# Kernel optimization log

Measured on AMD Instinct MI355X. Metric: run time of the kernel, lower is better.

Reference implementation:

```python
import jax, jax.numpy as jnp
import numpy as np

B = 4            # batch
L = 4096         # max_len
D_MODEL = 1024   # qkv_dim == out_features
H = 16           # num_heads
SEG = 64         # max_seg_len
HD = D_MODEL // H          # head_dim = 64
NSEG = L // SEG            # num segments = 64
NEG = -1e10


def setup_inputs() -> dict:
    key = jax.random.key(0)
    k0, k1, k2, k3, k4 = jax.random.split(key, 5)
    scale = 1.0 / np.sqrt(D_MODEL).astype(np.float32)
    x = jax.random.normal(k0, (B, L, D_MODEL), jnp.float32)
    wq = jax.random.normal(k1, (D_MODEL, H, HD), jnp.float32) * scale
    wk = jax.random.normal(k2, (D_MODEL, H, HD), jnp.float32) * scale
    wv = jax.random.normal(k3, (D_MODEL, H, HD), jnp.float32) * scale
    wo = jax.random.normal(k4, (H, HD, D_MODEL), jnp.float32) * scale
    return {"input_qkv": x, "wq": wq, "wk": wk, "wv": wv, "wo": wo}


def reference(input_qkv, wq, wk, wv, wo):
    inv_sqrt_hd = 1.0 / np.sqrt(HD).astype(np.float32)
    # QKV projections; query pre-scaled by 1/sqrt(head_dim) as in get_qkv
    q = jnp.einsum('bld,dhf->blhf', input_qkv, wq) * inv_sqrt_hd
    k = jnp.einsum('bld,dhf->blhf', input_qkv, wk)
    v = jnp.einsum('bld,dhf->blhf', input_qkv, wv)

    cq = q.reshape(B * NSEG, SEG, H, HD)
    ck = k.reshape(B * NSEG, SEG, H, HD)
    cv = v.reshape(B * NSEG, SEG, H, HD)

    # Pooled per-segment query attends over its own segment's keys/values.
    # Original: merged_query = max(cq)*sqrt(HD), then flax dot_product_attention
    # rescales by 1/sqrt(HD) -> the two scalings cancel, so use max(cq) directly.
    mq = jnp.max(cq, axis=1, keepdims=True)                    # [B*NSEG, 1, H, HD]
    s_logits = jnp.einsum('bqhd,bkhd->bhqk', mq, ck)
    s_w = jax.nn.softmax(s_logits, axis=-1)
    s = jnp.einsum('bhqk,bkhd->bqhd', s_w, cv)                  # [B*NSEG, 1, H, HD]
    span_val = s.reshape(B, NSEG, H, HD)
    span_key = jnp.max(ck, axis=1).reshape(B, NSEG, H, HD)

    # Local causal attention logits within each segment
    causal = jnp.tril(jnp.ones((SEG, SEG), bool))
    local_bias = jnp.where(causal, 0.0, NEG).astype(jnp.float32)[None, :, None, :]
    local_logits = jnp.einsum('bqhd,bkhd->bqhk', cq, ck) + local_bias
    local_logits = local_logits.reshape(B, L, H, SEG)

    # Cross-segment logits: each token attends to strictly earlier segment summaries
    seg_id = jnp.arange(NSEG)
    prev_bias = jnp.where(seg_id[:, None] > seg_id[None, :], 0.0, NEG).astype(jnp.float32)
    prev_bias = jnp.repeat(prev_bias, SEG, axis=0)[None, :, None, :]  # [1, L, 1, NSEG]
    prev_logits = jnp.einsum('bqhd,bkhd->bqhk', q, span_key) + prev_bias

    # Joint softmax over [local keys | previous-segment summaries]
    joint = jnp.concatenate([local_logits, prev_logits], axis=-1)   # [B, L, H, SEG+NSEG]
    w = jax.nn.softmax(joint, axis=-1)
    local_att = w[..., :SEG].reshape(B * NSEG, SEG, H, SEG)
    prev_att = w[..., SEG:]

    local_merged = jnp.einsum('bqhk,bkhd->bqhd', local_att, cv).reshape(B, L, H, HD)
    prev_merged = jnp.einsum('bqhk,bkhd->bqhd', prev_att, span_val)

    return jnp.einsum('blhd,hdf->blf', local_merged + prev_merged, wo)
```

## Files before the change

### kernel.cpp

```cpp
#include <hip/hip_runtime.h>

#define BB    4
#define LL    4096
#define DM    1024
#define HH    16
#define SEGC  64
#define HDC   64
#define NSEGC 64
#define NEGV  -1.0e10f

typedef __bf16 bf16x8 __attribute__((ext_vector_type(8)));
typedef float  f32x4  __attribute__((ext_vector_type(4)));

__device__ __forceinline__ float bf2f(unsigned short s) {
  union { unsigned int u; float f; } x; x.u = ((unsigned int)s) << 16; return x.f;
}
__device__ __forceinline__ unsigned short f2bf(float f) {
  union { float f; unsigned int u; } x; x.f = f;
  unsigned int u = x.u;
  return (unsigned short)((u + 0x7fffu + ((u >> 16) & 1u)) >> 16);
}

__device__ __forceinline__ void gl2lds16(const unsigned short* g, unsigned short* l) {
  __builtin_amdgcn_global_load_lds(
      (const __attribute__((address_space(1))) unsigned int*)g,
      (__attribute__((address_space(3))) unsigned int*)l,
      16, 0, 0);
}

__device__ __forceinline__ void g2lds16(unsigned short* dst, const unsigned short* src) {
  int4 a = *(const int4*)(src);
  int4 b = *(const int4*)(src + 8);
  unsigned int* d = (unsigned int*)dst;
  const unsigned int* pa = (const unsigned int*)&a;
  const unsigned int* pb = (const unsigned int*)&b;
  d[0]=pa[0]; d[1]=pa[1]; d[2]=pa[2]; d[3]=pa[3];
  d[4]=pb[0]; d[5]=pb[1]; d[6]=pb[2]; d[7]=pb[3];
}

__global__ __launch_bounds__(256) void cvt_x(const float* __restrict__ x,
                                             unsigned short* __restrict__ xb) {
  const size_t i = ((size_t)blockIdx.x * 256 + threadIdx.x) * 8;
  float4 a = *(const float4*)(x + i);
  float4 b = *(const float4*)(x + i + 4);
  unsigned short o[8];
  o[0]=f2bf(a.x); o[1]=f2bf(a.y); o[2]=f2bf(a.z); o[3]=f2bf(a.w);
  o[4]=f2bf(b.x); o[5]=f2bf(b.y); o[6]=f2bf(b.z); o[7]=f2bf(b.w);
  *(int4*)(xb + i) = *(const int4*)o;
}

__global__ __launch_bounds__(256) void transpose_w(
    const float* __restrict__ wq, const float* __restrict__ wk,
    const float* __restrict__ wv, const float* __restrict__ wo,
    unsigned short* __restrict__ WqkvT, unsigned short* __restrict__ woT) {
  __shared__ unsigned short TS[64 * 65];

  const int z  = blockIdx.z;
  const int bx = blockIdx.x;
  const int by = blockIdx.y;
  const int t  = threadIdx.x;

  const float* src; unsigned short* dst; float scale = 1.0f;
  if (z == 0)      { src = wq; dst = WqkvT;               scale = 0.125f; }
  else if (z == 1) { src = wk; dst = WqkvT + 1024 * 1024; }
  else if (z == 2) { src = wv; dst = WqkvT + 2048 * 1024; }
  else             { src = wo; dst = woT; }

  const int rr = t >> 4;
  const int c4 = (t & 15) * 4;
  #pragma unroll
  for (int it = 0; it < 4; it++) {
    const int r = it * 16 + rr;
    float4 f = *(const float4*)(src + (size_t)(by * 64 + r) * 1024 + bx * 64 + c4);
    TS[(c4 + 0) * 65 + r] = f2bf(f.x * scale);
    TS[(c4 + 1) * 65 + r] = f2bf(f.y * scale);
    TS[(c4 + 2) * 65 + r] = f2bf(f.z * scale);
    TS[(c4 + 3) * 65 + r] = f2bf(f.w * scale);
  }
  __syncthreads();

  const int wr = t >> 3;
  const int w8 = (t & 7) * 8;
  #pragma unroll
  for (int it = 0; it < 2; it++) {
    const int n = it * 32 + wr;
    unsigned short o[8];
    #pragma unroll
    for (int j = 0; j < 8; j++) o[j] = TS[n * 65 + w8 + j];
    *(int4*)(dst + (size_t)(bx * 64 + n) * 1024 + by * 64 + w8) = *(const int4*)o;
  }
}

template <bool C_F32>
__global__ __launch_bounds__(512, 2) void gemm256(
    const unsigned short* __restrict__ A,
    const unsigned short* __restrict__ Bt,
    void* __restrict__ Cv,
    int ldc)
{
  __shared__ __align__(16) unsigned short L[2][2][4][4096];

  const int t    = threadIdx.x;
  const int wave = t >> 6;
  const int lane = t & 63;
  const int l15  = lane & 15;
  const int q4   = lane >> 4;
  const int wm   = wave >> 2;
  const int wn   = wave & 3;

  const int nwg = gridDim.x;
  const int wg  = blockIdx.x;
  const int swz = (wg & 7) * (nwg >> 3) + (wg >> 3);
  const int m0  = (swz & 63) << 8;
  const int n0  = (swz >> 6) << 8;

  const int srow = ((wave >> 1) << 4) + (lane >> 2);
  const int scol = ((wave & 1) << 5) + (((lane & 3) << 3) ^ (((lane >> 5) & 1) << 4));
  const size_t laneoff = (size_t)srow * 1024 + scol;
  const unsigned short* Ab = A  + (size_t)m0 * 1024 + laneoff;
  const unsigned short* Bb = Bt + (size_t)n0 * 1024 + laneoff;

  const int rdoff = l15 * 32 + ((q4 * 8) ^ (((l15 >> 3) & 1) << 4));

#define SA_(d, q, kt) gl2lds16(Ab + ((size_t)(q) * 64) * 1024 + (size_t)(kt) * 64, \
                               &L[d][0][q][0] + wave * 512)
#define SB_(d, q, kt) gl2lds16(Bb + ((size_t)(q) * 64) * 1024 + (size_t)(kt) * 64, \
                               &L[d][1][q][0] + wave * 512)
#define LDA8(d, i, kk) (*(const bf16x8*)(&L[d][0][wm * 2 + ((i) >> 2)][0] + \
                        ((((i) & 3) * 2 + (kk)) * 512) + rdoff))
#define LDB8(d, j, kk) (*(const bf16x8*)(&L[d][1][wn][0] + \
                        ((((j) * 2 + (kk))) * 512) + rdoff))
#define BAR()   asm volatile("s_barrier" ::: "memory")
#define VMW(n)  asm volatile("s_waitcnt vmcnt(" #n ")" ::: "memory")
#define MFMA_(av, bv, cv) __builtin_amdgcn_mfma_f32_16x16x32_bf16(av, bv, cv, 0, 0, 0)

  bf16x8 aLo[4][2], aHi[4][2], b01e[2][2], b01o[2][2], b23[2][2];

#define RD_ALO(d) { _Pragma("unroll") for (int ii = 0; ii < 4; ++ii) { \
    aLo[ii][0] = LDA8(d, ii, 0); aLo[ii][1] = LDA8(d, ii, 1); } }
#define RD_AHI(d) { _Pragma("unroll") for (int ii = 0; ii < 4; ++ii) { \
    aHi[ii][0] = LDA8(d, 4 + ii, 0); aHi[ii][1] = LDA8(d, 4 + ii, 1); } }
#define RD_B01(d, ARR) { _Pragma("unroll") for (int jj = 0; jj < 2; ++jj) { \
    ARR[jj][0] = LDB8(d, jj, 0); ARR[jj][1] = LDB8(d, jj, 1); } }
#define RD_B23(d) { _Pragma("unroll") for (int jj = 0; jj < 2; ++jj) { \
    b23[jj][0] = LDB8(d, 2 + jj, 0); b23[jj][1] = LDB8(d, 2 + jj, 1); } }

#define CL(AR, BR, IO, J0) do { \
    __builtin_amdgcn_sched_barrier(0); \
    __builtin_amdgcn_s_setprio(1); \
    _Pragma("unroll") for (int ii = 0; ii < 4; ++ii) { \
      _Pragma("unroll") for (int jj = 0; jj < 2; ++jj) { \
        acc[(IO) + ii][(J0) + jj] = MFMA_(AR[ii][0], BR[jj][0], acc[(IO) + ii][(J0) + jj]); \
        acc[(IO) + ii][(J0) + jj] = MFMA_(AR[ii][1], BR[jj][1], acc[(IO) + ii][(J0) + jj]); \
      } } \
    __builtin_amdgcn_s_setprio(0); } while (0)

  f32x4 acc[8][4];
  #pragma unroll
  for (int i = 0; i < 8; ++i)
    #pragma unroll
    for (int j = 0; j < 4; ++j) acc[i][j] = (f32x4){0.f, 0.f, 0.f, 0.f};

  SA_(0,0,0); SA_(0,2,0); SB_(0,0,0); SB_(0,1,0); SB_(0,2,0); SB_(0,3,0);
  SA_(0,1,0); SA_(0,3,0);
  SA_(1,0,1); SA_(1,2,1); SB_(1,0,1); SB_(1,1,1); SB_(1,2,1); SB_(1,3,1);
  SA_(1,1,1); SA_(1,3,1);
  VMW(8); BAR();
  RD_ALO(0); RD_B01(0, b01e);

  #pragma unroll 1
  for (int it = 0; it < 8; ++it) {
    const int t2 = (2 * it + 2) & 15;
    const int t3 = (2 * it + 3) & 15;

    RD_B23(0);
    SA_(0, 0, t2); SA_(0, 2, t2);
    CL(aLo, b01e, 0, 0);
    BAR();

    RD_AHI(0);
    SB_(0, 0, t2); SB_(0, 1, t2);
    CL(aLo, b23, 0, 2);
    BAR();

    SB_(0, 2, t2); SB_(0, 3, t2);
    CL(aHi, b23, 4, 2);
    VMW(6); BAR();

    RD_ALO(1); RD_B01(1, b01o);
    SA_(0, 1, t2); SA_(0, 3, t2);
    CL(aHi, b01e, 4, 0);
    BAR();

    RD_B23(1);
    SA_(1, 0, t3); SA_(1, 2, t3);
    CL(aLo, b01o, 0, 0);
    BAR();

    RD_AHI(1);
    SB_(1, 0, t3); SB_(1, 1, t3);
    CL(aLo, b23, 0, 2);
    BAR();

    SB_(1, 2, t3); SB_(1, 3, t3);
    CL(aHi, b23, 4, 2);
    VMW(6); BAR();

    RD_ALO(0); RD_B01(0, b01e);
    SA_(1, 1, t3); SA_(1, 3, t3);
    CL(aHi, b01o, 4, 0);
    BAR();
  }

  #pragma unroll
  for (int i = 0; i < 8; ++i) {
    #pragma unroll
    for (int j = 0; j < 4; ++j) {
      const int col = n0 + wn * 64 + j * 16 + l15;
      #pragma unroll
      for (int r = 0; r < 4; ++r) {
        const int row = m0 + wm * 128 + i * 16 + q4 * 4 + r;
        if (C_F32) ((float*)Cv)[(size_t)row * ldc + col] = acc[i][j][r];
        else ((unsigned short*)Cv)[(size_t)row * ldc + col] = f2bf(acc[i][j][r]);
      }
    }
  }
  VMW(0);

#undef SA_
#undef SB_
#undef LDA8
#undef LDB8
#undef BAR
#undef VMW
#undef MFMA_
#undef RD_ALO
#undef RD_AHI
#undef RD_B01
#undef RD_B23
#undef CL
}

__global__ __launch_bounds__(64) void span_kernel(
    const unsigned short* __restrict__ qkv,
    unsigned short* __restrict__ spanK,
    unsigned short* __restrict__ spanV)
{
  __shared__ unsigned short QS[64 * 66], KS[64 * 66], VS[64 * 66];
  __shared__ float mqs[64], ws[64];

  const int c = blockIdx.x;
  const int h = blockIdx.y;
  const int b = c >> 6, n = c & 63;
  const int t = threadIdx.x;

  const size_t rowbase = ((size_t)(b * LL + n * SEGC + t)) * 3072 + h * 64;
  #pragma unroll
  for (int j = 0; j < 4; j++) {
    g2lds16(QS + t * 66 + j * 16, qkv + rowbase + j * 16);
    g2lds16(KS + t * 66 + j * 16, qkv + rowbase + 1024 + j * 16);
    g2lds16(VS + t * 66 + j * 16, qkv + rowbase + 2048 + j * 16);
  }
  __syncthreads();

  float mqa = -3.0e38f, mqb = -3.0e38f, ska = -3.0e38f, skc = -3.0e38f;
  #pragma unroll 8
  for (int r = 0; r < 64; r += 2) {
    mqa = fmaxf(mqa, bf2f(QS[r * 66 + t]));
    mqb = fmaxf(mqb, bf2f(QS[(r + 1) * 66 + t]));
    ska = fmaxf(ska, bf2f(KS[r * 66 + t]));
    skc = fmaxf(skc, bf2f(KS[(r + 1) * 66 + t]));
  }
  mqs[t] = fmaxf(mqa, mqb);
  spanK[((size_t)c * 16 + h) * 64 + t] = f2bf(fmaxf(ska, skc));
  __syncthreads();

  float l0 = 0.f, l1 = 0.f;
  #pragma unroll 8
  for (int d = 0; d < 64; d += 2) {
    l0 += mqs[d] * bf2f(KS[t * 66 + d]);
    l1 += mqs[d + 1] * bf2f(KS[t * 66 + d + 1]);
  }
  float logit = l0 + l1;
  float m = logit;
  #pragma unroll
  for (int off = 32; off; off >>= 1) m = fmaxf(m, __shfl_xor(m, off, 64));
  float e = __expf(logit - m);
  float s = e;
  #pragma unroll
  for (int off = 32; off; off >>= 1) s += __shfl_xor(s, off, 64);
  ws[t] = e / s;
  __syncthreads();

  float sv0 = 0.f, sv1 = 0.f;
  #pragma unroll 8
  for (int kk = 0; kk < 64; kk += 2) {
    sv0 += ws[kk] * bf2f(VS[kk * 66 + t]);
    sv1 += ws[kk + 1] * bf2f(VS[(kk + 1) * 66 + t]);
  }
  spanV[((size_t)c * 16 + h) * 64 + t] = f2bf(sv0 + sv1);
}

__global__ __launch_bounds__(256) void attn_kernel(
    const unsigned short* __restrict__ qkv,
    const unsigned short* __restrict__ spanK,
    const unsigned short* __restrict__ spanV,
    unsigned short* __restrict__ att)
{
  __shared__ unsigned short VT[64 * 136];
  __shared__ unsigned short WL[64 * 136];

  const int c = blockIdx.x;
  const int h = blockIdx.y;
  const int b = c >> 6, n = c & 63;
  const int t = threadIdx.x;
  const int wave = t >> 6;
  const int lane = t & 63;
  const int l15  = lane & 15;
  const int q4   = lane >> 4;

  #pragma unroll
  for (int it = 0; it < 4; it++) {
    const int idx = t + 256 * it;
    const int kp  = idx >> 3;
    const int fc  = (idx & 7) * 8;
    const unsigned short* src;
    if (kp < 64)
      src = qkv + ((size_t)(b * LL + n * SEGC + kp)) * 3072 + 2048 + h * 64 + fc;
    else
      src = spanV + ((size_t)(b * 64 + (kp - 64)) * 16 + h) * 64 + fc;
    int4 val = *(const int4*)src;
    const unsigned short* e = (const unsigned short*)&val;
    const int kb = kp >> 3;
    #pragma unroll
    for (int i = 0; i < 8; i++) {
      const int f  = fc + i;
      const int nb = (kb & 8) | ((kb ^ (f >> 3)) & 7);
      VT[f * 136 + nb * 8 + (kp & 7)] = e[i];
    }
  }

  bf16x8 af[2];
  {
    const size_t qbase = ((size_t)(b * LL + n * SEGC + wave * 16 + l15)) * 3072
                         + h * 64 + q4 * 8;
    af[0] = *(const bf16x8*)(qkv + qbase);
    af[1] = *(const bf16x8*)(qkv + qbase + 32);
  }

  f32x4 accl[8];
  #pragma unroll
  for (int tt = 0; tt < 8; tt++) accl[tt] = (f32x4){0.f, 0.f, 0.f, 0.f};

  #pragma unroll
  for (int s = 0; s < 2; s++) {
    bf16x8 bfr[8];
    #pragma unroll
    for (int tt = 0; tt < 8; tt++) {
      const unsigned short* src;
      if (tt < 4)
        src = qkv + ((size_t)(b * LL + n * SEGC + tt * 16 + l15)) * 3072
              + 1024 + h * 64 + s * 32 + q4 * 8;
      else
        src = spanK + ((size_t)((b * 64 + (tt - 4) * 16 + l15) * 16 + h)) * 64
              + s * 32 + q4 * 8;
      bfr[tt] = *(const bf16x8*)src;
    }
    #pragma unroll
    for (int tt = 0; tt < 8; tt++)
      accl[tt] = __builtin_amdgcn_mfma_f32_16x16x32_bf16(af[s], bfr[tt], accl[tt], 0, 0, 0);
  }

  #pragma unroll
  for (int tt = 0; tt < 8; tt++) {
    const int col = (tt & 3) * 16 + l15;
    #pragma unroll
    for (int rr = 0; rr < 4; rr++) {
      const int r_att = wave * 16 + q4 * 4 + rr;
      const bool valid = (tt < 4) ? (col <= r_att) : (col < n);
      if (!valid) accl[tt][rr] = NEGV;
    }
  }

  #pragma unroll
  for (int rr = 0; rr < 4; rr++) {
    float mx = accl[0][rr];
    #pragma unroll
    for (int tt = 1; tt < 8; tt++) mx = fmaxf(mx, accl[tt][rr]);
    #pragma unroll
    for (int msk = 1; msk < 16; msk <<= 1) mx = fmaxf(mx, __shfl_xor(mx, msk, 64));
    float sm = 0.f;
    float ex[8];
    #pragma unroll
    for (int tt = 0; tt < 8; tt++) { ex[tt] = __expf(accl[tt][rr] - mx); sm += ex[tt]; }
    #pragma unroll
    for (int msk = 1; msk < 16; msk <<= 1) sm += __shfl_xor(sm, msk, 64);
    const float inv = 1.0f / sm;
    const int r_att = wave * 16 + q4 * 4 + rr;
    #pragma unroll
    for (int tt = 0; tt < 8; tt++) {
      const int colj = (tt < 4) ? (tt * 16 + l15) : (64 + (tt - 4) * 16 + l15);
      WL[r_att * 136 + colj] = f2bf(ex[tt] * inv);
    }
  }

  __syncthreads();

  f32x4 accm[4];
  #pragma unroll
  for (int j = 0; j < 4; j++) accm[j] = (f32x4){0.f, 0.f, 0.f, 0.f};
  #pragma unroll
  for (int s = 0; s < 4; s++) {
    const bf16x8 aw = *(const bf16x8*)(WL + (wave * 16 + l15) * 136 + s * 32 + q4 * 8);
    #pragma unroll
    for (int j = 0; j < 4; j++) {
      const int f  = j * 16 + l15;
      const int kb = s * 4 + q4;
      const int nb = (kb & 8) | ((kb ^ (f >> 3)) & 7);
      const bf16x8 bv = *(const bf16x8*)(VT + f * 136 + nb * 8);
      accm[j] = __builtin_amdgcn_mfma_f32_16x16x32_bf16(aw, bv, accm[j], 0, 0, 0);
    }
  }

  #pragma unroll
  for (int j = 0; j < 4; j++) {
    #pragma unroll
    for (int rr = 0; rr < 4; rr++) {
      const int row = wave * 16 + q4 * 4 + rr;
      const int col = j * 16 + l15;
      att[((size_t)(b * LL + n * SEGC + row)) * 1024 + h * 64 + col] = f2bf(accm[j][rr]);
    }
  }
}

extern "C" void kernel_launch(void* const* d_in, const int* in_sizes, int n_in,
                              void* d_out, int out_size, void* d_ws, size_t ws_size,
                              hipStream_t stream) {
  const float* x  = (const float*)d_in[0];
  const float* wq = (const float*)d_in[1];
  const float* wk = (const float*)d_in[2];
  const float* wv = (const float*)d_in[3];
  const float* wo = (const float*)d_in[4];
  float* out = (float*)d_out;

  unsigned short* wsp   = (unsigned short*)d_ws;
  unsigned short* xb    = wsp;
  unsigned short* qkv   = xb + 16777216;
  unsigned short* WqkvT = qkv + 50331648;
  unsigned short* woT   = WqkvT + 3145728;
  unsigned short* skb   = woT + 1048576;
  unsigned short* svb   = skb + 262144;
  unsigned short* attb  = xb;

  cvt_x<<<8192, 256, 0, stream>>>(x, xb);
  transpose_w<<<dim3(16, 16, 4), 256, 0, stream>>>(wq, wk, wv, wo, WqkvT, woT);
  gemm256<false><<<768, 512, 0, stream>>>(xb, WqkvT, (void*)qkv, 3072);
  span_kernel<<<dim3(256, 16), 64, 0, stream>>>(qkv, skb, svb);
  attn_kernel<<<dim3(256, 16), 256, 0, stream>>>(qkv, skb, svb, attb);
  gemm256<true><<<256, 512, 0, stream>>>(attb, woT, (void*)out, 1024);
}
```

Before: 346.4 us.

## Retile GEMMs to 128x256 blocks and stage attention keys in LDS

Replaces the 256x256, BK=64 hand-scheduled GEMM with a 128x256 tile using BK=32, a simple double-buffered loop and an XCD-aware block mapping. This doubles the grid for both the QKV and output projections, aiming at better CU fill, especially for the small output GEMM. The trade-off is less data reuse per tile and more barriers per unit of work. Separately, the attention kernel now loads segment keys and span keys into a padded LDS buffer once, instead of each wave issuing strided global loads for its MFMA operands.

```diff
diff --git a/kernel.cpp b/kernel.cpp
--- a/kernel.cpp
+++ b/kernel.cpp
@@ -92,13 +92,14 @@
 }
 
 template <bool C_F32>
-__global__ __launch_bounds__(512, 2) void gemm256(
+__global__ __launch_bounds__(512, 4) void gemm128x256(
     const unsigned short* __restrict__ A,
     const unsigned short* __restrict__ Bt,
     void* __restrict__ Cv,
     int ldc)
 {
-  __shared__ __align__(16) unsigned short L[2][2][4][4096];
+  __shared__ __align__(16) unsigned short LA[2][8][512];
+  __shared__ __align__(16) unsigned short LB[2][16][512];
 
   const int t    = threadIdx.x;
   const int wave = t >> 6;
@@ -108,118 +109,76 @@
   const int wm   = wave >> 2;
   const int wn   = wave & 3;
 
-  const int nwg = gridDim.x;
   const int wg  = blockIdx.x;
-  const int swz = (wg & 7) * (nwg >> 3) + (wg >> 3);
-  const int m0  = (swz & 63) << 8;
-  const int n0  = (swz >> 6) << 8;
-
-  const int srow = ((wave >> 1) << 4) + (lane >> 2);
-  const int scol = ((wave & 1) << 5) + (((lane & 3) << 3) ^ (((lane >> 5) & 1) << 4));
-  const size_t laneoff = (size_t)srow * 1024 + scol;
-  const unsigned short* Ab = A  + (size_t)m0 * 1024 + laneoff;
-  const unsigned short* Bb = Bt + (size_t)n0 * 1024 + laneoff;
+  const int xcd = wg & 7;
+  const int r_  = wg >> 3;
+  const int lm  = r_ & 15;
+  const int nt  = r_ >> 4;
+  const int m0  = ((xcd << 4) + lm) << 7;
+  const int n0  = nt << 8;
+
+  const int srow = lane >> 2;
+  const int scol = ((lane & 3) << 3) ^ (((lane >> 5) & 1) << 4);
+  const unsigned short* Abase = A  + (size_t)(m0 + wave * 16 + srow) * 1024 + scol;
+  const unsigned short* Bbase = Bt + (size_t)(n0 + wave * 16 + srow) * 1024 + scol;
 
   const int rdoff = l15 * 32 + ((q4 * 8) ^ (((l15 >> 3) & 1) << 4));
 
-#define SA_(d, q, kt) gl2lds16(Ab + ((size_t)(q) * 64) * 1024 + (size_t)(kt) * 64, \
-                               &L[d][0][q][0] + wave * 512)
-#define SB_(d, q, kt) gl2lds16(Bb + ((size_t)(q) * 64) * 1024 + (size_t)(kt) * 64, \
-                               &L[d][1][q][0] + wave * 512)
-#define LDA8(d, i, kk) (*(const bf16x8*)(&L[d][0][wm * 2 + ((i) >> 2)][0] + \
-                        ((((i) & 3) * 2 + (kk)) * 512) + rdoff))
-#define LDB8(d, j, kk) (*(const bf16x8*)(&L[d][1][wn][0] + \
-                        ((((j) * 2 + (kk))) * 512) + rdoff))
+#define SA_(d, kt)  gl2lds16(Abase + (size_t)(kt) * 32, &LA[d][wave][0])
+#define SB0_(d, kt) gl2lds16(Bbase + (size_t)(kt) * 32, &LB[d][wave][0])
+#define SB1_(d, kt) gl2lds16(Bbase + (size_t)128 * 1024 + (size_t)(kt) * 32, \
+                             &LB[d][8 + wave][0])
+#define LDA8(d, i) (*(const bf16x8*)(&LA[d][wm * 4 + (i)][0] + rdoff))
+#define LDB8(d, j) (*(const bf16x8*)(&LB[d][wn * 4 + (j)][0] + rdoff))
 #define BAR()   asm volatile("s_barrier" ::: "memory")
+#define LGKM0() asm volatile("s_waitcnt lgkmcnt(0)" ::: "memory")
 #define VMW(n)  asm volatile("s_waitcnt vmcnt(" #n ")" ::: "memory")
 #define MFMA_(av, bv, cv) __builtin_amdgcn_mfma_f32_16x16x32_bf16(av, bv, cv, 0, 0, 0)
 
-  bf16x8 aLo[4][2], aHi[4][2], b01e[2][2], b01o[2][2], b23[2][2];
-
-#define RD_ALO(d) { _Pragma("unroll") for (int ii = 0; ii < 4; ++ii) { \
-    aLo[ii][0] = LDA8(d, ii, 0); aLo[ii][1] = LDA8(d, ii, 1); } }
-#define RD_AHI(d) { _Pragma("unroll") for (int ii = 0; ii < 4; ++ii) { \
-    aHi[ii][0] = LDA8(d, 4 + ii, 0); aHi[ii][1] = LDA8(d, 4 + ii, 1); } }
-#define RD_B01(d, ARR) { _Pragma("unroll") for (int jj = 0; jj < 2; ++jj) { \
-    ARR[jj][0] = LDB8(d, jj, 0); ARR[jj][1] = LDB8(d, jj, 1); } }
-#define RD_B23(d) { _Pragma("unroll") for (int jj = 0; jj < 2; ++jj) { \
-    b23[jj][0] = LDB8(d, 2 + jj, 0); b23[jj][1] = LDB8(d, 2 + jj, 1); } }
-
-#define CL(AR, BR, IO, J0) do { \
-    __builtin_amdgcn_sched_barrier(0); \
-    __builtin_amdgcn_s_setprio(1); \
-    _Pragma("unroll") for (int ii = 0; ii < 4; ++ii) { \
-      _Pragma("unroll") for (int jj = 0; jj < 2; ++jj) { \
-        acc[(IO) + ii][(J0) + jj] = MFMA_(AR[ii][0], BR[jj][0], acc[(IO) + ii][(J0) + jj]); \
-        acc[(IO) + ii][(J0) + jj] = MFMA_(AR[ii][1], BR[jj][1], acc[(IO) + ii][(J0) + jj]); \
-      } } \
-    __builtin_amdgcn_s_setprio(0); } while (0)
-
-  f32x4 acc[8][4];
-  #pragma unroll
-  for (int i = 0; i < 8; ++i)
+  f32x4 acc[4][4];
+  #pragma unroll
+  for (int i = 0; i < 4; ++i)
     #pragma unroll
     for (int j = 0; j < 4; ++j) acc[i][j] = (f32x4){0.f, 0.f, 0.f, 0.f};
 
-  SA_(0,0,0); SA_(0,2,0); SB_(0,0,0); SB_(0,1,0); SB_(0,2,0); SB_(0,3,0);
-  SA_(0,1,0); SA_(0,3,0);
-  SA_(1,0,1); SA_(1,2,1); SB_(1,0,1); SB_(1,1,1); SB_(1,2,1); SB_(1,3,1);
-  SA_(1,1,1); SA_(1,3,1);
-  VMW(8); BAR();
-  RD_ALO(0); RD_B01(0, b01e);
+  SA_(0, 0); SB0_(0, 0); SB1_(0, 0);
+  SA_(1, 1); SB0_(1, 1); SB1_(1, 1);
+  VMW(3); BAR();
 
   #pragma unroll 1
-  for (int it = 0; it < 8; ++it) {
-    const int t2 = (2 * it + 2) & 15;
-    const int t3 = (2 * it + 3) & 15;
-
-    RD_B23(0);
-    SA_(0, 0, t2); SA_(0, 2, t2);
-    CL(aLo, b01e, 0, 0);
+  for (int it = 0; it < 32; ++it) {
+    const int cur = it & 1;
+    const int nxt = (it + 2) & 31;
+
+    bf16x8 a[4], b[4];
+    #pragma unroll
+    for (int i = 0; i < 4; ++i) a[i] = LDA8(cur, i);
+    #pragma unroll
+    for (int j = 0; j < 4; ++j) b[j] = LDB8(cur, j);
+    LGKM0();
     BAR();
-
-    RD_AHI(0);
-    SB_(0, 0, t2); SB_(0, 1, t2);
-    CL(aLo, b23, 0, 2);
+    SA_(cur, nxt); SB0_(cur, nxt); SB1_(cur, nxt);
+
+    __builtin_amdgcn_s_setprio(1);
+    #pragma unroll
+    for (int i = 0; i < 4; ++i)
+      #pragma unroll
+      for (int j = 0; j < 4; ++j)
+        acc[i][j] = MFMA_(a[i], b[j], acc[i][j]);
+    __builtin_amdgcn_s_setprio(0);
+
+    VMW(3);
     BAR();
-
-    SB_(0, 2, t2); SB_(0, 3, t2);
-    CL(aHi, b23, 4, 2);
-    VMW(6); BAR();
-
-    RD_ALO(1); RD_B01(1, b01o);
-    SA_(0, 1, t2); SA_(0, 3, t2);
-    CL(aHi, b01e, 4, 0);
-    BAR();
-
-    RD_B23(1);
-    SA_(1, 0, t3); SA_(1, 2, t3);
-    CL(aLo, b01o, 0, 0);
-    BAR();
-
-    RD_AHI(1);
-    SB_(1, 0, t3); SB_(1, 1, t3);
-    CL(aLo, b23, 0, 2);
-    BAR();
-
-    SB_(1, 2, t3); SB_(1, 3, t3);
-    CL(aHi, b23, 4, 2);
-    VMW(6); BAR();
-
-    RD_ALO(0); RD_B01(0, b01e);
-    SA_(1, 1, t3); SA_(1, 3, t3);
-    CL(aHi, b01o, 4, 0);
-    BAR();
-  }
-
-  #pragma unroll
-  for (int i = 0; i < 8; ++i) {
+  }
+
+  #pragma unroll
+  for (int i = 0; i < 4; ++i) {
     #pragma unroll
     for (int j = 0; j < 4; ++j) {
       const int col = n0 + wn * 64 + j * 16 + l15;
       #pragma unroll
       for (int r = 0; r < 4; ++r) {
-        const int row = m0 + wm * 128 + i * 16 + q4 * 4 + r;
+        const int row = m0 + wm * 64 + i * 16 + q4 * 4 + r;
         if (C_F32) ((float*)Cv)[(size_t)row * ldc + col] = acc[i][j][r];
         else ((unsigned short*)Cv)[(size_t)row * ldc + col] = f2bf(acc[i][j][r]);
       }
@@ -228,17 +187,14 @@
   VMW(0);
 
 #undef SA_
-#undef SB_
+#undef SB0_
+#undef SB1_
 #undef LDA8
 #undef LDB8
 #undef BAR
+#undef LGKM0
 #undef VMW
 #undef MFMA_
-#undef RD_ALO
-#undef RD_AHI
-#undef RD_B01
-#undef RD_B23
-#undef CL
 }
 
 __global__ __launch_bounds__(64) void span_kernel(
@@ -307,8 +263,9 @@
     const unsigned short* __restrict__ spanV,
     unsigned short* __restrict__ att)
 {
-  __shared__ unsigned short VT[64 * 136];
-  __shared__ unsigned short WL[64 * 136];
+  __shared__ __align__(16) unsigned short KJ[128 * 72];
+  __shared__ __align__(16) unsigned short VT[64 * 136];
+  __shared__ __align__(16) unsigned short WL[64 * 136];
 
   const int c = blockIdx.x;
   const int h = blockIdx.y;
@@ -318,6 +275,15 @@
   const int lane = t & 63;
   const int l15  = lane & 15;
   const int q4   = lane >> 4;
+
+  {
+    const int r  = t >> 2;
+    const int qq = (t & 3) * 16;
+    g2lds16(KJ + r * 72 + qq,
+            qkv + ((size_t)(b * LL + n * SEGC + r)) * 3072 + 1024 + h * 64 + qq);
+    g2lds16(KJ + (64 + r) * 72 + qq,
+            spanK + ((size_t)(b * 64 + r) * 16 + h) * 64 + qq);
+  }
 
   #pragma unroll
   for (int it = 0; it < 4; it++) {
@@ -348,6 +314,8 @@
     af[1] = *(const bf16x8*)(qkv + qbase + 32);
   }
 
+  __syncthreads();
+
   f32x4 accl[8];
   #pragma unroll
   for (int tt = 0; tt < 8; tt++) accl[tt] = (f32x4){0.f, 0.f, 0.f, 0.f};
@@ -356,16 +324,8 @@
   for (int s = 0; s < 2; s++) {
     bf16x8 bfr[8];
     #pragma unroll
-    for (int tt = 0; tt < 8; tt++) {
-      const unsigned short* src;
-      if (tt < 4)
-        src = qkv + ((size_t)(b * LL + n * SEGC + tt * 16 + l15)) * 3072
-              + 1024 + h * 64 + s * 32 + q4 * 8;
-      else
-        src = spanK + ((size_t)((b * 64 + (tt - 4) * 16 + l15) * 16 + h)) * 64
-              + s * 32 + q4 * 8;
-      bfr[tt] = *(const bf16x8*)src;
-    }
+    for (int tt = 0; tt < 8; tt++)
+      bfr[tt] = *(const bf16x8*)(KJ + (tt * 16 + l15) * 72 + s * 32 + q4 * 8);
     #pragma unroll
     for (int tt = 0; tt < 8; tt++)
       accl[tt] = __builtin_amdgcn_mfma_f32_16x16x32_bf16(af[s], bfr[tt], accl[tt], 0, 0, 0);
@@ -454,8 +414,8 @@
 
   cvt_x<<<8192, 256, 0, stream>>>(x, xb);
   transpose_w<<<dim3(16, 16, 4), 256, 0, stream>>>(wq, wk, wv, wo, WqkvT, woT);
-  gemm256<false><<<768, 512, 0, stream>>>(xb, WqkvT, (void*)qkv, 3072);
+  gemm128x256<false><<<1536, 512, 0, stream>>>(xb, WqkvT, (void*)qkv, 3072);
   span_kernel<<<dim3(256, 16), 64, 0, stream>>>(qkv, skb, svb);
   attn_kernel<<<dim3(256, 16), 256, 0, stream>>>(qkv, skb, svb, attb);
-  gemm256<true><<<256, 512, 0, stream>>>(attb, woT, (void*)out, 1024);
-}
+  gemm128x256<true><<<512, 512, 0, stream>>>(attb, woT, (void*)out, 1024);
+}
```

Result: faster. 337.5 us (-2.6%).
